# Kernel optimization log

Measured on AMD Instinct MI355X. Metric: run time of the kernel, lower is better.

## Reference

```python
import jax, jax.numpy as jnp
import numpy as np

# Human3.6M skeleton: 16 bones over 17 joints
SKELETON = [(0,1),(1,2),(2,3),(0,4),(4,5),(5,6),(0,7),(7,8),(8,9),(9,10),(8,11),(11,12),(12,13),(8,14),(14,15),(15,16)]
PARENT = jnp.array([p for p, c in SKELETON], dtype=jnp.int32)
CHILD = jnp.array([c for p, c in SKELETON], dtype=jnp.int32)
NUM_BONES = 16
EPS = 1e-9


def setup_inputs() -> dict:
    key = jax.random.key(0)
    k1, k2, k3, k4, k5 = jax.random.split(key, 5)
    B, J = 1000000, 17
    pred_jts = jax.random.normal(k1, (B, J, 3), dtype=jnp.float32)
    gt_bl = jax.random.uniform(k2, (B, NUM_BONES), dtype=jnp.float32)
    anchor_scores = jax.random.uniform(k3, (B, J), dtype=jnp.float32)
    # ShiftAttention params: fc1 (32->16), fc2 (16->32), no bias; stored as [in, out]
    W1 = jax.random.normal(k4, (2 * NUM_BONES, NUM_BONES), dtype=jnp.float32) * (2.0 / (2 * NUM_BONES)) ** 0.5
    W2 = jax.random.normal(k5, (NUM_BONES, 2 * NUM_BONES), dtype=jnp.float32) * (2.0 / NUM_BONES) ** 0.5
    return {"pred_jts": pred_jts, "gt_bl": gt_bl, "anchor_scores": anchor_scores, "W1": W1, "W2": W2}


def reference(pred_jts, gt_bl, anchor_scores, W1, W2):
    B = pred_jts.shape[0]
    # per-edge gather: bone vectors [B, 16, 3]
    diff = pred_jts[:, PARENT, :] - pred_jts[:, CHILD, :]
    bl_norm = jnp.linalg.norm(diff, axis=-1)            # [B, 16]
    dis_bl = gt_bl - bl_norm                            # bone-length error
    a_p = anchor_scores[:, PARENT]
    a_c = anchor_scores[:, CHILD]
    a_sum = a_p + a_c + EPS
    # split correction between parent (weighted by child score) and child
    move_bl = jnp.stack([dis_bl * a_c / a_sum, dis_bl * a_p / a_sum], axis=-1)  # [B, 16, 2]
    # ShiftAttention gate: sigmoid(relu(x W1) W2)
    x = move_bl.reshape(B, 2 * NUM_BONES)
    gate = jax.nn.sigmoid(jax.nn.relu(x @ W1) @ W2).reshape(B, NUM_BONES, 2)
    move_bl = move_bl * gate
    # unit bone directions and per-edge forces
    unit = diff / (bl_norm[..., None] + EPS)            # [B, 16, 3]
    force_parent = move_bl[..., 0:1] * unit
    force_child = -move_bl[..., 1:2] * unit
    # scatter-add forces into joints (duplicate joint indices accumulate)
    move_jts = jnp.zeros_like(pred_jts).at[:, PARENT].add(force_parent).at[:, CHILD].add(force_child)
    return pred_jts + move_jts
```

## Files before the change

kernel.cpp:

```cpp
#include <hip/hip_runtime.h>

#define DEV __device__ __forceinline__

typedef __fp16 h16x2 __attribute__((ext_vector_type(2)));

DEV void gload_lds16(const void* g, void* lds) {
    __builtin_amdgcn_global_load_lds(
        (const __attribute__((address_space(1))) void*)g,
        (__attribute__((address_space(3))) void*)lds,
        16, 0, 0);
}

DEV float dot2(h16x2 a, h16x2 b, float acc) {
    asm("v_dot2_f32_f16 %0, %1, %2, %0" : "+v"(acc) : "v"(a), "v"(b));
    return acc;
}

DEV h16x2 f2h(float a, float b) { return __builtin_amdgcn_cvt_pkrtz(a, b); }

DEV float fast_sigmoid(float v) {
    return __builtin_amdgcn_rcpf(1.0f + __builtin_amdgcn_exp2f(-1.4426950408889634f * v));
}

#define SKEL_TABLES \
    constexpr int PAR[16] = {0,1,2,0,4,5,0,7,8,9,8,11,12,8,14,15}; \
    constexpr int CHI[16] = {1,2,3,4,5,6,7,8,9,10,11,12,13,14,15,16};

DEV void compute_sample(const float (&p)[51], const float (&a)[17], const float (&g)[16],
                        const float4* sW1h4, const float4* sW2h4, float (&o)[51])
{
    SKEL_TABLES

    float x[32], invn[16];
    #pragma unroll
    for (int k = 0; k < 16; ++k) {
        const int P = PAR[k] * 3, C = CHI[k] * 3;
        const float dx = p[P]   - p[C];
        const float dy = p[P+1] - p[C+1];
        const float dz = p[P+2] - p[C+2];
        const float n  = __builtin_amdgcn_sqrtf(fmaf(dx,dx, fmaf(dy,dy, dz*dz)));
        const float dis = g[k] - n;
        const float ap = a[PAR[k]], ac = a[CHI[k]];
        const float inv_asum = __builtin_amdgcn_rcpf(ap + ac + 1e-9f);
        x[2*k]   = dis * ac * inv_asum;
        x[2*k+1] = dis * ap * inv_asum;
        invn[k]  = __builtin_amdgcn_rcpf(n + 1e-9f);
    }

    h16x2 xp[16];
    #pragma unroll
    for (int ip = 0; ip < 16; ++ip) xp[ip] = f2h(x[2*ip], x[2*ip+1]);

    float y[16];
    #pragma unroll
    for (int j = 0; j < 16; ++j) y[j] = 0.f;
    #pragma unroll
    for (int ip = 0; ip < 16; ++ip) {
        #pragma unroll
        for (int jj = 0; jj < 4; ++jj) {
            const float4 wq = sW1h4[ip*4 + jj];
            y[4*jj+0] = dot2(xp[ip], __builtin_bit_cast(h16x2, wq.x), y[4*jj+0]);
            y[4*jj+1] = dot2(xp[ip], __builtin_bit_cast(h16x2, wq.y), y[4*jj+1]);
            y[4*jj+2] = dot2(xp[ip], __builtin_bit_cast(h16x2, wq.z), y[4*jj+2]);
            y[4*jj+3] = dot2(xp[ip], __builtin_bit_cast(h16x2, wq.w), y[4*jj+3]);
        }
    }
    h16x2 hp[8];
    #pragma unroll
    for (int jp = 0; jp < 8; ++jp)
        hp[jp] = f2h(fmaxf(y[2*jp], 0.f), fmaxf(y[2*jp+1], 0.f));

    float gg[32];
    #pragma unroll
    for (int c = 0; c < 32; ++c) gg[c] = 0.f;
    #pragma unroll
    for (int jp = 0; jp < 8; ++jp) {
        #pragma unroll
        for (int cc = 0; cc < 8; ++cc) {
            const float4 wq = sW2h4[jp*8 + cc];
            gg[4*cc+0] = dot2(hp[jp], __builtin_bit_cast(h16x2, wq.x), gg[4*cc+0]);
            gg[4*cc+1] = dot2(hp[jp], __builtin_bit_cast(h16x2, wq.y), gg[4*cc+1]);
            gg[4*cc+2] = dot2(hp[jp], __builtin_bit_cast(h16x2, wq.z), gg[4*cc+2]);
            gg[4*cc+3] = dot2(hp[jp], __builtin_bit_cast(h16x2, wq.w), gg[4*cc+3]);
        }
    }

    float xg[32];
    #pragma unroll
    for (int c = 0; c < 32; ++c) xg[c] = x[c] * fast_sigmoid(gg[c]);
    #pragma unroll
    for (int k = 0; k < 16; ++k) {
        xg[2*k]   *= invn[k];
        xg[2*k+1] *= invn[k];
    }

    #pragma unroll
    for (int j = 0; j < 17; ++j) {
        float ox = p[3*j], oy = p[3*j+1], oz = p[3*j+2];
        #pragma unroll
        for (int k = 0; k < 16; ++k) {
            if (PAR[k] == j || CHI[k] == j) {
                const int P = PAR[k] * 3, C = CHI[k] * 3;
                const float dx = p[P]   - p[C];
                const float dy = p[P+1] - p[C+1];
                const float dz = p[P+2] - p[C+2];
                const float s = (PAR[k] == j) ? xg[2*k] : -xg[2*k+1];
                ox = fmaf(s, dx, ox);
                oy = fmaf(s, dy, oy);
                oz = fmaf(s, dz, oz);
            }
        }
        o[3*j]   = ox;
        o[3*j+1] = oy;
        o[3*j+2] = oz;
    }
}

DEV void compute_sample_f32(const float (&p)[51], const float (&a)[17], const float (&g)[16],
                            const float* __restrict__ gW1, const float* __restrict__ gW2,
                            float (&o)[51])
{
    SKEL_TABLES

    float x[32], invn[16];
    #pragma unroll
    for (int k = 0; k < 16; ++k) {
        const int P = PAR[k] * 3, C = CHI[k] * 3;
        const float dx = p[P]   - p[C];
        const float dy = p[P+1] - p[C+1];
        const float dz = p[P+2] - p[C+2];
        const float n  = __builtin_amdgcn_sqrtf(fmaf(dx,dx, fmaf(dy,dy, dz*dz)));
        const float dis = g[k] - n;
        const float ap = a[PAR[k]], ac = a[CHI[k]];
        const float inv_asum = __builtin_amdgcn_rcpf(ap + ac + 1e-9f);
        x[2*k]   = dis * ac * inv_asum;
        x[2*k+1] = dis * ap * inv_asum;
        invn[k]  = __builtin_amdgcn_rcpf(n + 1e-9f);
    }

    float y[16];
    #pragma unroll
    for (int j = 0; j < 16; ++j) y[j] = 0.f;
    for (int i = 0; i < 32; ++i) {
        const float xi = x[i];
        #pragma unroll
        for (int j = 0; j < 16; ++j) y[j] = fmaf(xi, gW1[i*16 + j], y[j]);
    }
    float h[16];
    #pragma unroll
    for (int j = 0; j < 16; ++j) h[j] = fmaxf(y[j], 0.f);

    float gg[32];
    #pragma unroll
    for (int c = 0; c < 32; ++c) gg[c] = 0.f;
    for (int j = 0; j < 16; ++j) {
        const float hj = h[j];
        #pragma unroll
        for (int c = 0; c < 32; ++c) gg[c] = fmaf(hj, gW2[j*32 + c], gg[c]);
    }

    float xg[32];
    #pragma unroll
    for (int c = 0; c < 32; ++c) xg[c] = x[c] * fast_sigmoid(gg[c]);
    #pragma unroll
    for (int k = 0; k < 16; ++k) {
        xg[2*k]   *= invn[k];
        xg[2*k+1] *= invn[k];
    }

    #pragma unroll
    for (int j = 0; j < 17; ++j) {
        float ox = p[3*j], oy = p[3*j+1], oz = p[3*j+2];
        #pragma unroll
        for (int k = 0; k < 16; ++k) {
            if (PAR[k] == j || CHI[k] == j) {
                const int P = PAR[k] * 3, C = CHI[k] * 3;
                const float dx = p[P]   - p[C];
                const float dy = p[P+1] - p[C+1];
                const float dz = p[P+2] - p[C+2];
                const float s = (PAR[k] == j) ? xg[2*k] : -xg[2*k+1];
                ox = fmaf(s, dx, ox);
                oy = fmaf(s, dy, oy);
                oz = fmaf(s, dz, oz);
            }
        }
        o[3*j]   = ox;
        o[3*j+1] = oy;
        o[3*j+2] = oz;
    }
}

__global__ __launch_bounds__(64, 2) void projts_kernel(
    const float* __restrict__ pred,
    const float* __restrict__ gt,
    const float* __restrict__ anc,
    const float* __restrict__ gW1,
    const float* __restrict__ gW2,
    float* __restrict__ out,
    int B)
{
    constexpr int ROW = 51;
    constexpr int WBUF = 64 * ROW;
    constexpr int WOFF1 = 1536;
    constexpr int WOFF2 = 1792;

    __shared__ float sbuf[WBUF] __attribute__((aligned(16)));

    const int l = threadIdx.x;
    float* buf  = sbuf;
    float4* buf4 = reinterpret_cast<float4*>(buf);

    const long long wavebase = (long long)blockIdx.x * 64;

    if (wavebase + 64 <= (long long)B) {
        float p[51], a[17], o[51];

        const char* srcB = reinterpret_cast<const char*>(pred + (size_t)wavebase * ROW);
        char* bufB = reinterpret_cast<char*>(buf);

        #pragma unroll
        for (int i = 0; i < 12; ++i)
            gload_lds16(srcB + (size_t)(i*64 + l)*16, bufB + i*1024);
        if (l < 48)
            gload_lds16(srcB + (size_t)(768 + l)*16, bufB + 12*1024);

        const float4* asrc4 = reinterpret_cast<const float4*>(anc + (size_t)wavebase * 17);
        float4 ar0 = asrc4[0*64 + l];
        float4 ar1 = asrc4[1*64 + l];
        float4 ar2 = asrc4[2*64 + l];
        float4 ar3 = asrc4[3*64 + l];
        float4 ar4 = asrc4[256 + (l & 15)];

        const float4* gsrc4 = reinterpret_cast<const float4*>(gt + (size_t)(wavebase + l) * 16);
        const float4 gq0 = gsrc4[0], gq1 = gsrc4[1], gq2 = gsrc4[2], gq3 = gsrc4[3];

        float w1a[4], w1b[4], w2a[4], w2b[4];
        #pragma unroll
        for (int q = 0; q < 4; ++q) {
            const int t4 = l + 64*q;
            const int ip = t4 >> 4, j = t4 & 15;
            w1a[q] = gW1[32*ip + j];
            w1b[q] = gW1[32*ip + 16 + j];
            const int jp = t4 >> 5, c = t4 & 31;
            w2a[q] = gW2[64*jp + c];
            w2b[q] = gW2[64*jp + 32 + c];
        }

        __syncthreads();

        #pragma unroll
        for (int j = 0; j < ROW; ++j) p[j] = buf[l*ROW + j];

        __syncthreads();

        buf4[0*64 + l] = ar0;
        buf4[1*64 + l] = ar1;
        buf4[2*64 + l] = ar2;
        buf4[3*64 + l] = ar3;
        buf4[256 + l]  = ar4;
        #pragma unroll
        for (int q = 0; q < 4; ++q) {
            buf[WOFF1 + l + 64*q] = __builtin_bit_cast(float, f2h(w1a[q], w1b[q]));
            buf[WOFF2 + l + 64*q] = __builtin_bit_cast(float, f2h(w2a[q], w2b[q]));
        }

        __syncthreads();

        #pragma unroll
        for (int j = 0; j < 17; ++j) a[j] = buf[l*17 + j];

        __syncthreads();

        const float g[16] = {gq0.x,gq0.y,gq0.z,gq0.w, gq1.x,gq1.y,gq1.z,gq1.w,
                             gq2.x,gq2.y,gq2.z,gq2.w, gq3.x,gq3.y,gq3.z,gq3.w};

        const float4* sW1h4 = reinterpret_cast<const float4*>(buf + WOFF1);
        const float4* sW2h4 = reinterpret_cast<const float4*>(buf + WOFF2);
        compute_sample(p, a, g, sW1h4, sW2h4, o);

        #pragma unroll
        for (int j = 0; j < ROW; ++j) buf[l*ROW + j] = o[j];

        __syncthreads();

        float4* dst4 = reinterpret_cast<float4*>(out + (size_t)wavebase * ROW);
        #pragma unroll
        for (int i = 0; i < 12; ++i) dst4[i*64 + l] = buf4[i*64 + l];
        if (l < 48) dst4[768 + l] = buf4[768 + l];
    } else {
        const long long b = wavebase + l;
        if (b < B) {
            float p[51], a[17], g[16], o[51];
            const float* pj = pred + (size_t)b * 51;
            #pragma unroll
            for (int j = 0; j < 51; ++j) p[j] = pj[j];
            const float* ab = anc + (size_t)b * 17;
            #pragma unroll
            for (int j = 0; j < 17; ++j) a[j] = ab[j];
            const float* gb = gt + (size_t)b * 16;
            #pragma unroll
            for (int j = 0; j < 16; ++j) g[j] = gb[j];

            compute_sample_f32(p, a, g, gW1, gW2, o);

            float* ob = out + (size_t)b * 51;
            #pragma unroll
            for (int j = 0; j < 51; ++j) ob[j] = o[j];
        }
    }
}

extern "C" void kernel_launch(void* const* d_in, const int* in_sizes, int n_in,
                              void* d_out, int out_size, void* d_ws, size_t ws_size,
                              hipStream_t stream) {
    const float* pred = (const float*)d_in[0];
    const float* gt   = (const float*)d_in[1];
    const float* anc  = (const float*)d_in[2];
    const float* W1   = (const float*)d_in[3];
    const float* W2   = (const float*)d_in[4];
    float* out = (float*)d_out;

    const int B = in_sizes[0] / 51;
    const int blocks = (B + 63) / 64;
    hipLaunchKernelGGL(projts_kernel, dim3(blocks), dim3(64), 0, stream,
                       pred, gt, anc, W1, W2, out, B);
}
```

Before: 103.1 us.

## Make blocks persistent over five chunks with double-buffered async LDS prefetch

Each block now handles five 64-sample chunks instead of one. Pred and anchor loads for the next chunk are double-buffered into LDS through global_load_lds, and gt is prefetched into registers, with explicit vmcnt/lgkmcnt waits so loads overlap compute. The fp16 weight staging is done once per block rather than once per chunk, and the anchor path now goes straight to LDS. The hand-tuned waitcnt counts and the larger LDS footprint add correctness risk and may lower occupancy.

```diff
diff --git a/kernel.cpp b/kernel.cpp
--- a/kernel.cpp
+++ b/kernel.cpp
@@ -3,6 +3,11 @@
 #define DEV __device__ __forceinline__
 
 typedef __fp16 h16x2 __attribute__((ext_vector_type(2)));
+
+#define WAIT_VM(N)  do { asm volatile("s_waitcnt vmcnt(" #N ")" ::: "memory"); \
+                         __builtin_amdgcn_sched_barrier(0); } while (0)
+#define WAIT_LGKM() do { asm volatile("s_waitcnt lgkmcnt(0)" ::: "memory"); \
+                         __builtin_amdgcn_sched_barrier(0); } while (0)
 
 DEV void gload_lds16(const void* g, void* lds) {
     __builtin_amdgcn_global_load_lds(
@@ -190,120 +195,133 @@
     }
 }
 
-__global__ __launch_bounds__(64, 2) void projts_kernel(
+__global__ __launch_bounds__(64) void projts_kernel(
     const float* __restrict__ pred,
     const float* __restrict__ gt,
     const float* __restrict__ anc,
     const float* __restrict__ gW1,
     const float* __restrict__ gW2,
     float* __restrict__ out,
-    int B)
+    int B, int g1)
 {
-    constexpr int ROW = 51;
-    constexpr int WBUF = 64 * ROW;
-    constexpr int WOFF1 = 1536;
-    constexpr int WOFF2 = 1792;
-
-    __shared__ float sbuf[WBUF] __attribute__((aligned(16)));
-
-    const int l = threadIdx.x;
-    float* buf  = sbuf;
-    float4* buf4 = reinterpret_cast<float4*>(buf);
-
-    const long long wavebase = (long long)blockIdx.x * 64;
-
-    if (wavebase + 64 <= (long long)B) {
-        float p[51], a[17], o[51];
-
-        const char* srcB = reinterpret_cast<const char*>(pred + (size_t)wavebase * ROW);
-        char* bufB = reinterpret_cast<char*>(buf);
-
-        #pragma unroll
-        for (int i = 0; i < 12; ++i)
-            gload_lds16(srcB + (size_t)(i*64 + l)*16, bufB + i*1024);
-        if (l < 48)
-            gload_lds16(srcB + (size_t)(768 + l)*16, bufB + 12*1024);
-
-        const float4* asrc4 = reinterpret_cast<const float4*>(anc + (size_t)wavebase * 17);
-        float4 ar0 = asrc4[0*64 + l];
-        float4 ar1 = asrc4[1*64 + l];
-        float4 ar2 = asrc4[2*64 + l];
-        float4 ar3 = asrc4[3*64 + l];
-        float4 ar4 = asrc4[256 + (l & 15)];
-
-        const float4* gsrc4 = reinterpret_cast<const float4*>(gt + (size_t)(wavebase + l) * 16);
-        const float4 gq0 = gsrc4[0], gq1 = gsrc4[1], gq2 = gsrc4[2], gq3 = gsrc4[3];
-
-        float w1a[4], w1b[4], w2a[4], w2b[4];
-        #pragma unroll
-        for (int q = 0; q < 4; ++q) {
-            const int t4 = l + 64*q;
-            const int ip = t4 >> 4, j = t4 & 15;
-            w1a[q] = gW1[32*ip + j];
-            w1b[q] = gW1[32*ip + 16 + j];
-            const int jp = t4 >> 5, c = t4 & 31;
-            w2a[q] = gW2[64*jp + c];
-            w2b[q] = gW2[64*jp + 32 + c];
-        }
-
-        __syncthreads();
-
-        #pragma unroll
-        for (int j = 0; j < ROW; ++j) p[j] = buf[l*ROW + j];
-
-        __syncthreads();
-
-        buf4[0*64 + l] = ar0;
-        buf4[1*64 + l] = ar1;
-        buf4[2*64 + l] = ar2;
-        buf4[3*64 + l] = ar3;
-        buf4[256 + l]  = ar4;
-        #pragma unroll
-        for (int q = 0; q < 4; ++q) {
-            buf[WOFF1 + l + 64*q] = __builtin_bit_cast(float, f2h(w1a[q], w1b[q]));
-            buf[WOFF2 + l + 64*q] = __builtin_bit_cast(float, f2h(w2a[q], w2b[q]));
-        }
-
-        __syncthreads();
-
-        #pragma unroll
-        for (int j = 0; j < 17; ++j) a[j] = buf[l*17 + j];
-
-        __syncthreads();
-
-        const float g[16] = {gq0.x,gq0.y,gq0.z,gq0.w, gq1.x,gq1.y,gq1.z,gq1.w,
-                             gq2.x,gq2.y,gq2.z,gq2.w, gq3.x,gq3.y,gq3.z,gq3.w};
-
-        const float4* sW1h4 = reinterpret_cast<const float4*>(buf + WOFF1);
-        const float4* sW2h4 = reinterpret_cast<const float4*>(buf + WOFF2);
-        compute_sample(p, a, g, sW1h4, sW2h4, o);
-
-        #pragma unroll
-        for (int j = 0; j < ROW; ++j) buf[l*ROW + j] = o[j];
-
-        __syncthreads();
-
-        float4* dst4 = reinterpret_cast<float4*>(out + (size_t)wavebase * ROW);
-        #pragma unroll
-        for (int i = 0; i < 12; ++i) dst4[i*64 + l] = buf4[i*64 + l];
-        if (l < 48) dst4[768 + l] = buf4[768 + l];
+    constexpr int ROW  = 51;
+    constexpr int PBUF = 64 * ROW;
+    constexpr int ABUF = 64 * 17;
+    constexpr int CPB  = 5;
+
+    __shared__ float pb[2][PBUF] __attribute__((aligned(16)));
+    __shared__ float ab[2][ABUF] __attribute__((aligned(16)));
+    __shared__ float wb[512]     __attribute__((aligned(16)));
+
+    const int l   = threadIdx.x;
+    const int bid = blockIdx.x;
+
+    if (bid < g1) {
+        const long long c0 = (long long)bid * CPB;
+
+        {
+            float w1a[4], w1b[4], w2a[4], w2b[4];
+            #pragma unroll
+            for (int q = 0; q < 4; ++q) {
+                const int t4 = l + 64*q;
+                const int ip = t4 >> 4, j = t4 & 15;
+                w1a[q] = gW1[32*ip + j];
+                w1b[q] = gW1[32*ip + 16 + j];
+                const int jp = t4 >> 5, c = t4 & 31;
+                w2a[q] = gW2[64*jp + c];
+                w2b[q] = gW2[64*jp + 32 + c];
+            }
+            #pragma unroll
+            for (int q = 0; q < 4; ++q) {
+                wb[l + 64*q]       = __builtin_bit_cast(float, f2h(w1a[q], w1b[q]));
+                wb[256 + l + 64*q] = __builtin_bit_cast(float, f2h(w2a[q], w2b[q]));
+            }
+        }
+        const float4* sW1h4 = reinterpret_cast<const float4*>(wb);
+        const float4* sW2h4 = reinterpret_cast<const float4*>(wb + 256);
+
+        auto issue = [&](int k, int side) {
+            const long long base = (c0 + k) * 64;
+            const char* srcB = reinterpret_cast<const char*>(pred + (size_t)base * ROW);
+            char* pB = reinterpret_cast<char*>(pb[side]);
+            #pragma unroll
+            for (int i = 0; i < 12; ++i)
+                gload_lds16(srcB + (size_t)(i*64 + l)*16, pB + i*1024);
+            if (l < 48)
+                gload_lds16(srcB + (size_t)(768 + l)*16, pB + 12*1024);
+            const char* aB = reinterpret_cast<const char*>(anc + (size_t)base * 17);
+            char* abB = reinterpret_cast<char*>(ab[side]);
+            #pragma unroll
+            for (int i = 0; i < 4; ++i)
+                gload_lds16(aB + (size_t)(i*64 + l)*16, abB + i*1024);
+            if (l < 16)
+                gload_lds16(aB + (size_t)(256 + l)*16, abB + 4*1024);
+        };
+
+        float4 gtA0, gtA1, gtA2, gtA3, gtB0, gtB1, gtB2, gtB3;
+        auto loadgt = [&](int k, int side) {
+            const float4* gs = reinterpret_cast<const float4*>(
+                gt + (size_t)((c0 + k) * 64 + l) * 16);
+            if (side == 0) { gtA0 = gs[0]; gtA1 = gs[1]; gtA2 = gs[2]; gtA3 = gs[3]; }
+            else           { gtB0 = gs[0]; gtB1 = gs[1]; gtB2 = gs[2]; gtB3 = gs[3]; }
+        };
+
+        issue(0, 0); loadgt(0, 0);
+        issue(1, 1); loadgt(1, 1);
+
+        for (int k = 0; k < CPB; ++k) {
+            const int cur = k & 1;
+            float* pbc = pb[cur];
+            float* abc = ab[cur];
+
+            if (k < CPB - 1) { WAIT_VM(22); } else { WAIT_VM(0); }
+
+            float p[51], a17[17];
+            #pragma unroll
+            for (int j = 0; j < ROW; ++j) p[j] = pbc[l*ROW + j];
+            #pragma unroll
+            for (int j = 0; j < 17; ++j) a17[j] = abc[l*17 + j];
+            WAIT_LGKM();
+
+            float4 q0, q1, q2, q3;
+            if (cur == 0) { q0 = gtA0; q1 = gtA1; q2 = gtA2; q3 = gtA3; }
+            else          { q0 = gtB0; q1 = gtB1; q2 = gtB2; q3 = gtB3; }
+            const float g[16] = {q0.x,q0.y,q0.z,q0.w, q1.x,q1.y,q1.z,q1.w,
+                                 q2.x,q2.y,q2.z,q2.w, q3.x,q3.y,q3.z,q3.w};
+
+            float o[51];
+            compute_sample(p, a17, g, sW1h4, sW2h4, o);
+
+            #pragma unroll
+            for (int j = 0; j < ROW; ++j) pbc[l*ROW + j] = o[j];
+            WAIT_LGKM();
+
+            float4* dst4 = reinterpret_cast<float4*>(out + (size_t)(c0 + k) * 64 * ROW);
+            const float4* pb4 = reinterpret_cast<const float4*>(pbc);
+            #pragma unroll
+            for (int i = 0; i < 12; ++i) dst4[i*64 + l] = pb4[i*64 + l];
+            if (l < 48) dst4[768 + l] = pb4[768 + l];
+            WAIT_LGKM();
+
+            if (k + 2 < CPB) { issue(k + 2, cur); loadgt(k + 2, cur); }
+        }
     } else {
-        const long long b = wavebase + l;
-        if (b < B) {
+        const long long s = (long long)g1 * CPB * 64 + (long long)(bid - g1) * 64 + l;
+        if (s < B) {
             float p[51], a[17], g[16], o[51];
-            const float* pj = pred + (size_t)b * 51;
+            const float* pj = pred + (size_t)s * 51;
             #pragma unroll
             for (int j = 0; j < 51; ++j) p[j] = pj[j];
-            const float* ab = anc + (size_t)b * 17;
-            #pragma unroll
-            for (int j = 0; j < 17; ++j) a[j] = ab[j];
-            const float* gb = gt + (size_t)b * 16;
+            const float* abp = anc + (size_t)s * 17;
+            #pragma unroll
+            for (int j = 0; j < 17; ++j) a[j] = abp[j];
+            const float* gb = gt + (size_t)s * 16;
             #pragma unroll
             for (int j = 0; j < 16; ++j) g[j] = gb[j];
 
             compute_sample_f32(p, a, g, gW1, gW2, o);
 
-            float* ob = out + (size_t)b * 51;
+            float* ob = out + (size_t)s * 51;
             #pragma unroll
             for (int j = 0; j < 51; ++j) ob[j] = o[j];
         }
@@ -321,7 +339,12 @@
     float* out = (float*)d_out;
 
     const int B = in_sizes[0] / 51;
-    const int blocks = (B + 63) / 64;
+    const int nchunk = B / 64;
+    const int g1 = nchunk / 5;
+    const long long covered = (long long)g1 * 5 * 64;
+    const int tail_blocks = (int)((B - covered + 63) / 64);
+    const int blocks = g1 + tail_blocks;
+
     hipLaunchKernelGGL(projts_kernel, dim3(blocks), dim3(64), 0, stream,
-                       pred, gt, anc, W1, W2, out, B);
-}
+                       pred, gt, anc, W1, W2, out, B, g1);
+}
```

Result: slower. 178.3 us (+72.9%).
